# Performance work log

Measured on AMD Instinct MI355X. Metric: run time of the kernel, lower is better.

The kernel has to match this reference:

```python
import jax, jax.numpy as jnp
import numpy as np

T, S, F, A, POS = 32, 4096, 256, 64, 128


def setup_inputs() -> dict:
    key = jax.random.key(0)
    ks = jax.random.split(key, 12)
    sc = lambda fan_in: 1.0 / np.sqrt(fan_in)
    return {
        "batch_data": jax.random.normal(ks[0], (T * S, F), dtype=jnp.float32),
        "xywh": jax.random.uniform(ks[1], (T * S, 4), dtype=jnp.float32),
        # nn.Linear params (y = x @ W.T + b)
        "Wa": jax.random.uniform(ks[2], (A, F), minval=-sc(F), maxval=sc(F)),
        "ba": jax.random.uniform(ks[3], (A,), minval=-sc(F), maxval=sc(F)),
        "Wb": jax.random.uniform(ks[4], (A, F), minval=-sc(F), maxval=sc(F)),
        "bb": jax.random.uniform(ks[5], (A,), minval=-sc(F), maxval=sc(F)),
        "Wg": jax.random.uniform(ks[6], (F, F), minval=-sc(F), maxval=sc(F)),
        "bg": jax.random.uniform(ks[7], (F,), minval=-sc(F), maxval=sc(F)),
        "Wh": jax.random.uniform(ks[8], (POS, 2), minval=-sc(2), maxval=sc(2)),
        "bh": jax.random.uniform(ks[9], (POS,), minval=-sc(2), maxval=sc(2)),
    }


def reference(batch_data, xywh, Wa, ba, Wb, bb, Wg, bg, Wh, bh):
    x = batch_data.reshape(T, S, F)
    pos = xywh.reshape(T, S, -1)
    # positional embedding path (computed in original forward but unused in output)
    avg_pos = jnp.mean(pos, axis=0)            # [S, 4]
    rel_pos = pos[:, :, :2] - avg_pos[:, :2]   # [T, S, 2]
    _pos_embeds = rel_pos @ Wh.T + bh          # [T, S, POS] (dead, matches source)

    theta = x @ Wa.T + ba                      # [T, S, A]
    phi = x @ Wb.T + bb                        # [T, S, A]
    feats = x @ Wg.T + bg                      # [T, S, F]

    # per-object temporal attention: attn[s, t, u] = theta[t, s] . phi[u, s]
    attn = jnp.einsum('tsa,usa->stu', theta, phi)       # [S, T, T]
    out = jnp.einsum('stu,usf->tsf', attn, feats)       # [T, S, F]
    return out
```

## Files before the change

### kernel.cpp

```cpp
#include <hip/hip_runtime.h>

#define T_ 32
#define S_ 4096
#define F_ 256
#define A_ 64

typedef __attribute__((ext_vector_type(8))) short s8v;
typedef __attribute__((ext_vector_type(4))) float f4v;
typedef __attribute__((ext_vector_type(4))) short s4v;

#define MFMA(a, b, c) __builtin_amdgcn_mfma_f32_16x16x32_bf16((a), (b), (c), 0, 0, 0)

__device__ __forceinline__ unsigned short f2bf(float f) {
    unsigned int u = __builtin_bit_cast(unsigned int, f);
    u += 0x7FFFu + ((u >> 16) & 1u);
    return (unsigned short)(u >> 16);
}

__global__ void convert_weights(const float* __restrict__ Wa,
                                const float* __restrict__ Wb,
                                const float* __restrict__ Wg,
                                unsigned short* __restrict__ wsB)
{
    int base = (blockIdx.x * 256 + threadIdx.x) * 4;
    const float* src;
    if (base < 16384)      src = Wa + base;
    else if (base < 32768) src = Wb + (base - 16384);
    else                   src = Wg + (base - 32768);
    float4 v = *(const float4*)src;
    s4v p;
    p[0] = (short)f2bf(v.x); p[1] = (short)f2bf(v.y);
    p[2] = (short)f2bf(v.z); p[3] = (short)f2bf(v.w);
    *(s4v*)(wsB + base) = p;
}

#define XS_OFF 0
#define FT_OFF 16384
#define TH_OFF 32768
#define PH_OFF 36864
#define AT_OFF 40960
#define LDS_BYTES 43008

__global__ __launch_bounds__(256, 2) void fused_temporal(
    const float* __restrict__ X,
    const unsigned short* __restrict__ wsB,
    const float* __restrict__ ba, const float* __restrict__ bb,
    const float* __restrict__ bg,
    float* __restrict__ out)
{
    __shared__ alignas(16) unsigned char smem[LDS_BYTES];
    const int tid  = threadIdx.x;
    const int wave = tid >> 6;
    const int lane = tid & 63;
    const int quad = lane >> 4;
    const int l15  = lane & 15;
    const int s    = blockIdx.x;

    const unsigned short* WaB = wsB;
    const unsigned short* WbB = wsB + 16384;
    const unsigned short* WgB = wsB + 32768;

    #pragma unroll
    for (int i = 0; i < 4; ++i) {
        int linear = i * 256 + tid;
        int t = linear >> 5;
        int c = linear & 31;
        const float* xp = X + ((size_t)(t * S_ + s)) * F_ + c * 8;
        float4 v0 = *(const float4*)(xp);
        float4 v1 = *(const float4*)(xp + 4);
        s8v p;
        p[0] = (short)f2bf(v0.x); p[1] = (short)f2bf(v0.y);
        p[2] = (short)f2bf(v0.z); p[3] = (short)f2bf(v0.w);
        p[4] = (short)f2bf(v1.x); p[5] = (short)f2bf(v1.y);
        p[6] = (short)f2bf(v1.z); p[7] = (short)f2bf(v1.w);
        *(s8v*)(&smem[XS_OFF + t * 512 + (((c + t) & 31) << 4)]) = p;
    }
    __syncthreads();

    s8v afrag[2][8];
    #pragma unroll
    for (int mt = 0; mt < 2; ++mt) {
        int t = l15 + 16 * mt;
        #pragma unroll
        for (int ks = 0; ks < 8; ++ks) {
            int chunk = 4 * ks + quad;
            afrag[mt][ks] = *(const s8v*)(&smem[XS_OFF + t * 512 + (((chunk + t) & 31) << 4)]);
        }
    }

    {
        int n0 = 16 * wave;
        f4v ta0 = {0.f,0.f,0.f,0.f}, ta1 = {0.f,0.f,0.f,0.f};
        f4v pa0 = {0.f,0.f,0.f,0.f}, pa1 = {0.f,0.f,0.f,0.f};
        const unsigned short* wa_row = WaB + (size_t)(n0 + l15) * F_ + quad * 8;
        const unsigned short* wb_row = WbB + (size_t)(n0 + l15) * F_ + quad * 8;
        #pragma unroll
        for (int ks = 0; ks < 8; ++ks) {
            s8v bfa = *(const s8v*)(wa_row + ks * 32);
            s8v bfb = *(const s8v*)(wb_row + ks * 32);
            ta0 = MFMA(afrag[0][ks], bfa, ta0);
            ta1 = MFMA(afrag[1][ks], bfa, ta1);
            pa0 = MFMA(afrag[0][ks], bfb, pa0);
            pa1 = MFMA(afrag[1][ks], bfb, pa1);
        }
        float biasa = ba[n0 + l15];
        float biasb = bb[n0 + l15];
        int a_col = n0 + l15;
        int chunk = a_col >> 3;
        int sub   = (a_col & 7) * 2;
        #pragma unroll
        for (int mt = 0; mt < 2; ++mt) {
            f4v va = mt ? ta1 : ta0;
            f4v vb = mt ? pa1 : pa0;
            #pragma unroll
            for (int r = 0; r < 4; ++r) {
                int t  = quad * 4 + r + 16 * mt;
                int sw = ((chunk + t) & 7) << 4;
                *(unsigned short*)(&smem[TH_OFF + t * 128 + sw + sub]) = f2bf(va[r] + biasa);
                *(unsigned short*)(&smem[PH_OFF + t * 128 + sw + sub]) = f2bf(vb[r] + biasb);
            }
        }
    }

    #pragma unroll
    for (int g = 0; g < 4; ++g) {
        int n0 = 64 * wave + 16 * g;
        f4v fa0 = {0.f,0.f,0.f,0.f}, fa1 = {0.f,0.f,0.f,0.f};
        const unsigned short* wg_row = WgB + (size_t)(n0 + l15) * F_ + quad * 8;
        #pragma unroll
        for (int ks = 0; ks < 8; ++ks) {
            s8v bf = *(const s8v*)(wg_row + ks * 32);
            fa0 = MFMA(afrag[0][ks], bf, fa0);
            fa1 = MFMA(afrag[1][ks], bf, fa1);
        }
        float biasg = bg[n0 + l15];
        int f = n0 + l15;
        #pragma unroll
        for (int mt = 0; mt < 2; ++mt) {
            f4v v = mt ? fa1 : fa0;
            int u0 = quad * 4 + 16 * mt;
            s4v pk;
            #pragma unroll
            for (int r = 0; r < 4; ++r) pk[r] = (short)f2bf(v[r] + biasg);
            int addr = FT_OFF + f * 64 + ((((u0 >> 3) + f) & 3) << 4) + (u0 & 7) * 2;
            *(s4v*)(&smem[addr]) = pk;
        }
    }
    __syncthreads();

    {
        int mt = wave >> 1, nt = wave & 1;
        int t = l15 + 16 * mt;
        int u = l15 + 16 * nt;
        f4v acc = {0.f,0.f,0.f,0.f};
        #pragma unroll
        for (int ks = 0; ks < 2; ++ks) {
            int chunk = 4 * ks + quad;
            s8v av = *(const s8v*)(&smem[TH_OFF + t * 128 + (((chunk + t) & 7) << 4)]);
            s8v bv = *(const s8v*)(&smem[PH_OFF + u * 128 + (((chunk + u) & 7) << 4)]);
            acc = MFMA(av, bv, acc);
        }
        int chunk = u >> 3;
        int sub   = (u & 7) * 2;
        #pragma unroll
        for (int r = 0; r < 4; ++r) {
            int tt = quad * 4 + r + 16 * mt;
            *(unsigned short*)(&smem[AT_OFF + tt * 64 + (((chunk + tt) & 3) << 4) + sub]) = f2bf(acc[r]);
        }
    }
    __syncthreads();

    {
        s8v aa[2];
        #pragma unroll
        for (int mt = 0; mt < 2; ++mt) {
            int t = l15 + 16 * mt;
            aa[mt] = *(const s8v*)(&smem[AT_OFF + t * 64 + (((quad + t) & 3) << 4)]);
        }
        #pragma unroll
        for (int g = 0; g < 4; ++g) {
            int n0 = 64 * wave + 16 * g;
            int f  = n0 + l15;
            s8v bv = *(const s8v*)(&smem[FT_OFF + f * 64 + (((quad + f) & 3) << 4)]);
            #pragma unroll
            for (int mt = 0; mt < 2; ++mt) {
                f4v acc = {0.f,0.f,0.f,0.f};
                acc = MFMA(aa[mt], bv, acc);
                #pragma unroll
                for (int r = 0; r < 4; ++r) {
                    int t = quad * 4 + r + 16 * mt;
                    out[((size_t)(t * S_ + s)) * F_ + f] = acc[r];
                }
            }
        }
    }
}

extern "C" void kernel_launch(void* const* d_in, const int* in_sizes, int n_in,
                              void* d_out, int out_size, void* d_ws, size_t ws_size,
                              hipStream_t stream) {
    (void)in_sizes; (void)n_in; (void)ws_size; (void)out_size;
    const float* X  = (const float*)d_in[0];
    const float* Wa = (const float*)d_in[2];
    const float* ba = (const float*)d_in[3];
    const float* Wb = (const float*)d_in[4];
    const float* bb = (const float*)d_in[5];
    const float* Wg = (const float*)d_in[6];
    const float* bg = (const float*)d_in[7];
    float* out = (float*)d_out;
    unsigned short* wsB = (unsigned short*)d_ws;

    convert_weights<<<dim3(96), dim3(256), 0, stream>>>(Wa, Wb, Wg, wsB);
    fused_temporal<<<dim3(S_), dim3(256), 0, stream>>>(X, wsB, ba, bb, bg, out);
}
```

Measured before the change: 321.8 us.

## Make blocks persistent over 16 objects with register-resident weights and prefetched inputs

Each block now handles 16 consecutive objects instead of one, so the bf16 weight fragments for Wa, Wb and Wg are loaded into registers once per block rather than re-read from global memory for every object. The next object's fp32 input rows are prefetched into registers and written to a double-buffered LDS area while the current object computes, and the bf16 conversion of X now happens at fragment-read time. The trade-off is a large register and LDS footprint (about 107 KB LDS, one block per CU) and only 256 blocks, which may leave the GPU's CUs underfilled.

```diff
diff --git a/kernel.cpp b/kernel.cpp
--- a/kernel.cpp
+++ b/kernel.cpp
@@ -4,6 +4,8 @@
 #define S_ 4096
 #define F_ 256
 #define A_ 64
+#define G_ 16
+#define NBLK (S_ / G_)
 
 typedef __attribute__((ext_vector_type(8))) short s8v;
 typedef __attribute__((ext_vector_type(4))) float f4v;
@@ -15,6 +17,15 @@
     unsigned int u = __builtin_bit_cast(unsigned int, f);
     u += 0x7FFFu + ((u >> 16) & 1u);
     return (unsigned short)(u >> 16);
+}
+
+__device__ __forceinline__ s8v cvt8(float4 a, float4 b) {
+    s8v p;
+    p[0] = (short)f2bf(a.x); p[1] = (short)f2bf(a.y);
+    p[2] = (short)f2bf(a.z); p[3] = (short)f2bf(a.w);
+    p[4] = (short)f2bf(b.x); p[5] = (short)f2bf(b.y);
+    p[6] = (short)f2bf(b.z); p[7] = (short)f2bf(b.w);
+    return p;
 }
 
 __global__ void convert_weights(const float* __restrict__ Wa,
@@ -34,14 +45,15 @@
     *(s4v*)(wsB + base) = p;
 }
 
+#define XROW 1040
 #define XS_OFF 0
-#define FT_OFF 16384
-#define TH_OFF 32768
-#define PH_OFF 36864
-#define AT_OFF 40960
-#define LDS_BYTES 43008
-
-__global__ __launch_bounds__(256, 2) void fused_temporal(
+#define FT_OFF 66560
+#define TH_OFF 99328
+#define PH_OFF 103424
+#define AT_OFF 107520
+#define LDS_BYTES 109568
+
+__global__ __launch_bounds__(256, 1) void fused_temporal(
     const float* __restrict__ X,
     const unsigned short* __restrict__ wsB,
     const float* __restrict__ ba, const float* __restrict__ bb,
@@ -54,142 +66,162 @@
     const int lane = tid & 63;
     const int quad = lane >> 4;
     const int l15  = lane & 15;
-    const int s    = blockIdx.x;
-
-    const unsigned short* WaB = wsB;
-    const unsigned short* WbB = wsB + 16384;
-    const unsigned short* WgB = wsB + 32768;
-
+    const int s0   = blockIdx.x * G_;
+
+    s8v waF[8], wbF[8], wgF[4][8];
+    {
+        const unsigned short* wa_row = wsB         + (size_t)(16 * wave + l15) * F_ + quad * 8;
+        const unsigned short* wb_row = wsB + 16384 + (size_t)(16 * wave + l15) * F_ + quad * 8;
+        #pragma unroll
+        for (int ks = 0; ks < 8; ++ks) {
+            waF[ks] = *(const s8v*)(wa_row + ks * 32);
+            wbF[ks] = *(const s8v*)(wb_row + ks * 32);
+        }
+        #pragma unroll
+        for (int g = 0; g < 4; ++g) {
+            const unsigned short* wg_row = wsB + 32768 + (size_t)(64 * wave + 16 * g + l15) * F_ + quad * 8;
+            #pragma unroll
+            for (int ks = 0; ks < 8; ++ks) wgF[g][ks] = *(const s8v*)(wg_row + ks * 32);
+        }
+    }
+    const float biasa = ba[16 * wave + l15];
+    const float biasb = bb[16 * wave + l15];
+    float biasg[4];
     #pragma unroll
-    for (int i = 0; i < 4; ++i) {
-        int linear = i * 256 + tid;
-        int t = linear >> 5;
-        int c = linear & 31;
-        const float* xp = X + ((size_t)(t * S_ + s)) * F_ + c * 8;
-        float4 v0 = *(const float4*)(xp);
-        float4 v1 = *(const float4*)(xp + 4);
-        s8v p;
-        p[0] = (short)f2bf(v0.x); p[1] = (short)f2bf(v0.y);
-        p[2] = (short)f2bf(v0.z); p[3] = (short)f2bf(v0.w);
-        p[4] = (short)f2bf(v1.x); p[5] = (short)f2bf(v1.y);
-        p[6] = (short)f2bf(v1.z); p[7] = (short)f2bf(v1.w);
-        *(s8v*)(&smem[XS_OFF + t * 512 + (((c + t) & 31) << 4)]) = p;
+    for (int g = 0; g < 4; ++g) biasg[g] = bg[64 * wave + 16 * g + l15];
+
+    #pragma unroll
+    for (int r = 0; r < 8; ++r) {
+        int t = wave * 8 + r;
+        float4 v = *(const float4*)(X + ((size_t)(t * S_ + s0)) * F_ + lane * 4);
+        *(float4*)(&smem[XS_OFF + t * XROW + lane * 16]) = v;
     }
     __syncthreads();
 
-    s8v afrag[2][8];
-    #pragma unroll
-    for (int mt = 0; mt < 2; ++mt) {
-        int t = l15 + 16 * mt;
+    for (int i = 0; i < G_; ++i) {
+        const int p = i & 1;
+        const int s = s0 + i;
+        const int xb  = XS_OFF + p * (32 * XROW);
+        const int xbn = XS_OFF + (1 - p) * (32 * XROW);
+        const int ftb = FT_OFF + p * 16384;
+
+        float4 pf[8];
+        if (i + 1 < G_) {
+            #pragma unroll
+            for (int r = 0; r < 8; ++r) {
+                int t = wave * 8 + r;
+                pf[r] = *(const float4*)(X + ((size_t)(t * S_ + s + 1)) * F_ + lane * 4);
+            }
+        }
+
+        f4v ta0 = {0,0,0,0}, ta1 = {0,0,0,0}, pa0 = {0,0,0,0}, pa1 = {0,0,0,0};
+        f4v fa[4][2];
+        #pragma unroll
+        for (int g = 0; g < 4; ++g) { fa[g][0] = (f4v){0,0,0,0}; fa[g][1] = (f4v){0,0,0,0}; }
+
         #pragma unroll
         for (int ks = 0; ks < 8; ++ks) {
-            int chunk = 4 * ks + quad;
-            afrag[mt][ks] = *(const s8v*)(&smem[XS_OFF + t * 512 + (((chunk + t) & 31) << 4)]);
-        }
-    }
-
-    {
-        int n0 = 16 * wave;
-        f4v ta0 = {0.f,0.f,0.f,0.f}, ta1 = {0.f,0.f,0.f,0.f};
-        f4v pa0 = {0.f,0.f,0.f,0.f}, pa1 = {0.f,0.f,0.f,0.f};
-        const unsigned short* wa_row = WaB + (size_t)(n0 + l15) * F_ + quad * 8;
-        const unsigned short* wb_row = WbB + (size_t)(n0 + l15) * F_ + quad * 8;
-        #pragma unroll
-        for (int ks = 0; ks < 8; ++ks) {
-            s8v bfa = *(const s8v*)(wa_row + ks * 32);
-            s8v bfb = *(const s8v*)(wb_row + ks * 32);
-            ta0 = MFMA(afrag[0][ks], bfa, ta0);
-            ta1 = MFMA(afrag[1][ks], bfa, ta1);
-            pa0 = MFMA(afrag[0][ks], bfb, pa0);
-            pa1 = MFMA(afrag[1][ks], bfb, pa1);
-        }
-        float biasa = ba[n0 + l15];
-        float biasb = bb[n0 + l15];
-        int a_col = n0 + l15;
-        int chunk = a_col >> 3;
-        int sub   = (a_col & 7) * 2;
-        #pragma unroll
-        for (int mt = 0; mt < 2; ++mt) {
-            f4v va = mt ? ta1 : ta0;
-            f4v vb = mt ? pa1 : pa0;
-            #pragma unroll
-            for (int r = 0; r < 4; ++r) {
-                int t  = quad * 4 + r + 16 * mt;
-                int sw = ((chunk + t) & 7) << 4;
-                *(unsigned short*)(&smem[TH_OFF + t * 128 + sw + sub]) = f2bf(va[r] + biasa);
-                *(unsigned short*)(&smem[PH_OFF + t * 128 + sw + sub]) = f2bf(vb[r] + biasb);
-            }
-        }
-    }
-
-    #pragma unroll
-    for (int g = 0; g < 4; ++g) {
-        int n0 = 64 * wave + 16 * g;
-        f4v fa0 = {0.f,0.f,0.f,0.f}, fa1 = {0.f,0.f,0.f,0.f};
-        const unsigned short* wg_row = WgB + (size_t)(n0 + l15) * F_ + quad * 8;
-        #pragma unroll
-        for (int ks = 0; ks < 8; ++ks) {
-            s8v bf = *(const s8v*)(wg_row + ks * 32);
-            fa0 = MFMA(afrag[0][ks], bf, fa0);
-            fa1 = MFMA(afrag[1][ks], bf, fa1);
-        }
-        float biasg = bg[n0 + l15];
-        int f = n0 + l15;
-        #pragma unroll
-        for (int mt = 0; mt < 2; ++mt) {
-            f4v v = mt ? fa1 : fa0;
-            int u0 = quad * 4 + 16 * mt;
-            s4v pk;
-            #pragma unroll
-            for (int r = 0; r < 4; ++r) pk[r] = (short)f2bf(v[r] + biasg);
-            int addr = FT_OFF + f * 64 + ((((u0 >> 3) + f) & 3) << 4) + (u0 & 7) * 2;
-            *(s4v*)(&smem[addr]) = pk;
-        }
-    }
-    __syncthreads();
-
-    {
-        int mt = wave >> 1, nt = wave & 1;
-        int t = l15 + 16 * mt;
-        int u = l15 + 16 * nt;
-        f4v acc = {0.f,0.f,0.f,0.f};
-        #pragma unroll
-        for (int ks = 0; ks < 2; ++ks) {
-            int chunk = 4 * ks + quad;
-            s8v av = *(const s8v*)(&smem[TH_OFF + t * 128 + (((chunk + t) & 7) << 4)]);
-            s8v bv = *(const s8v*)(&smem[PH_OFF + u * 128 + (((chunk + u) & 7) << 4)]);
-            acc = MFMA(av, bv, acc);
-        }
-        int chunk = u >> 3;
-        int sub   = (u & 7) * 2;
-        #pragma unroll
-        for (int r = 0; r < 4; ++r) {
-            int tt = quad * 4 + r + 16 * mt;
-            *(unsigned short*)(&smem[AT_OFF + tt * 64 + (((chunk + tt) & 3) << 4) + sub]) = f2bf(acc[r]);
-        }
-    }
-    __syncthreads();
-
-    {
-        s8v aa[2];
-        #pragma unroll
-        for (int mt = 0; mt < 2; ++mt) {
-            int t = l15 + 16 * mt;
-            aa[mt] = *(const s8v*)(&smem[AT_OFF + t * 64 + (((quad + t) & 3) << 4)]);
-        }
-        #pragma unroll
-        for (int g = 0; g < 4; ++g) {
-            int n0 = 64 * wave + 16 * g;
-            int f  = n0 + l15;
-            s8v bv = *(const s8v*)(&smem[FT_OFF + f * 64 + (((quad + f) & 3) << 4)]);
+            s8v a0, a1;
+            {
+                const unsigned char* b0 = &smem[xb + l15 * XROW + ks * 128 + quad * 32];
+                a0 = cvt8(*(const float4*)(b0), *(const float4*)(b0 + 16));
+                const unsigned char* b1 = &smem[xb + (l15 + 16) * XROW + ks * 128 + quad * 32];
+                a1 = cvt8(*(const float4*)(b1), *(const float4*)(b1 + 16));
+            }
+            ta0 = MFMA(a0, waF[ks], ta0);
+            ta1 = MFMA(a1, waF[ks], ta1);
+            pa0 = MFMA(a0, wbF[ks], pa0);
+            pa1 = MFMA(a1, wbF[ks], pa1);
+            #pragma unroll
+            for (int g = 0; g < 4; ++g) {
+                fa[g][0] = MFMA(a0, wgF[g][ks], fa[g][0]);
+                fa[g][1] = MFMA(a1, wgF[g][ks], fa[g][1]);
+            }
+        }
+
+        {
+            int a_col = 16 * wave + l15;
+            int chunk = a_col >> 3;
+            int sub   = (a_col & 7) * 2;
             #pragma unroll
             for (int mt = 0; mt < 2; ++mt) {
-                f4v acc = {0.f,0.f,0.f,0.f};
-                acc = MFMA(aa[mt], bv, acc);
+                f4v va = mt ? ta1 : ta0;
+                f4v vb = mt ? pa1 : pa0;
                 #pragma unroll
                 for (int r = 0; r < 4; ++r) {
-                    int t = quad * 4 + r + 16 * mt;
-                    out[((size_t)(t * S_ + s)) * F_ + f] = acc[r];
+                    int t  = quad * 4 + r + 16 * mt;
+                    int sw = ((chunk + t) & 7) << 4;
+                    *(unsigned short*)(&smem[TH_OFF + t * 128 + sw + sub]) = f2bf(va[r] + biasa);
+                    *(unsigned short*)(&smem[PH_OFF + t * 128 + sw + sub]) = f2bf(vb[r] + biasb);
+                }
+            }
+        }
+        #pragma unroll
+        for (int g = 0; g < 4; ++g) {
+            int f = 64 * wave + 16 * g + l15;
+            #pragma unroll
+            for (int mt = 0; mt < 2; ++mt) {
+                f4v v = fa[g][mt];
+                int u0 = quad * 4 + 16 * mt;
+                s4v pk;
+                #pragma unroll
+                for (int r = 0; r < 4; ++r) pk[r] = (short)f2bf(v[r] + biasg[g]);
+                int addr = ftb + f * 64 + ((((u0 >> 3) + f) & 3) << 4) + (u0 & 7) * 2;
+                *(s4v*)(&smem[addr]) = pk;
+            }
+        }
+
+        if (i + 1 < G_) {
+            #pragma unroll
+            for (int r = 0; r < 8; ++r) {
+                int t = wave * 8 + r;
+                *(float4*)(&smem[xbn + t * XROW + lane * 16]) = pf[r];
+            }
+        }
+        __syncthreads();
+
+        {
+            int mt = wave >> 1, nt = wave & 1;
+            int t = l15 + 16 * mt;
+            int u = l15 + 16 * nt;
+            f4v acc = {0,0,0,0};
+            #pragma unroll
+            for (int ks = 0; ks < 2; ++ks) {
+                int chunk = 4 * ks + quad;
+                s8v av = *(const s8v*)(&smem[TH_OFF + t * 128 + (((chunk + t) & 7) << 4)]);
+                s8v bv = *(const s8v*)(&smem[PH_OFF + u * 128 + (((chunk + u) & 7) << 4)]);
+                acc = MFMA(av, bv, acc);
+            }
+            int chunk = u >> 3;
+            int sub   = (u & 7) * 2;
+            #pragma unroll
+            for (int r = 0; r < 4; ++r) {
+                int tt = quad * 4 + r + 16 * mt;
+                *(unsigned short*)(&smem[AT_OFF + tt * 64 + (((chunk + tt) & 3) << 4) + sub]) = f2bf(acc[r]);
+            }
+        }
+        __syncthreads();
+
+        {
+            s8v aa[2];
+            #pragma unroll
+            for (int mt = 0; mt < 2; ++mt) {
+                int t = l15 + 16 * mt;
+                aa[mt] = *(const s8v*)(&smem[AT_OFF + t * 64 + (((quad + t) & 3) << 4)]);
+            }
+            #pragma unroll
+            for (int g = 0; g < 4; ++g) {
+                int f = 64 * wave + 16 * g + l15;
+                s8v bv = *(const s8v*)(&smem[ftb + f * 64 + (((quad + f) & 3) << 4)]);
+                #pragma unroll
+                for (int mt = 0; mt < 2; ++mt) {
+                    f4v acc = {0,0,0,0};
+                    acc = MFMA(aa[mt], bv, acc);
+                    #pragma unroll
+                    for (int r = 0; r < 4; ++r) {
+                        int t = quad * 4 + r + 16 * mt;
+                        out[((size_t)(t * S_ + s)) * F_ + f] = acc[r];
+                    }
                 }
             }
         }
@@ -211,5 +243,5 @@
     unsigned short* wsB = (unsigned short*)d_ws;
 
     convert_weights<<<dim3(96), dim3(256), 0, stream>>>(Wa, Wb, Wg, wsB);
-    fused_temporal<<<dim3(S_), dim3(256), 0, stream>>>(X, wsB, ba, bb, bg, out);
-}
+    fused_temporal<<<dim3(NBLK), dim3(256), 0, stream>>>(X, wsB, ba, bb, bg, out);
+}
```

Result: slower. 355.1 us (+10.3%).
